# Performance work log

Hardware: AMD Instinct MI355X
Metric: run time of the kernel (lower is better)

## Reference

```python
import jax, jax.numpy as jnp
import numpy as np

INPUT_SIZE = 512
HIDDEN = 1024
N_QP = 64
M_QP = 128
QP_ITER = 50
MIN_EIG = 0.01
N_P = N_QP * (N_QP + 1) // 2              # 2080
N_H = M_QP * N_QP                          # 8192
N_OUT = N_P + N_QP + N_H + M_QP            # 10464
BATCH = 1024


def setup_inputs() -> dict:
    key = jax.random.key(0)
    ks = jax.random.split(key, 4)
    s = lambda fan_in: np.float32(1.0 / np.sqrt(fan_in))
    return {
        "x": jax.random.normal(ks[0], (BATCH, INPUT_SIZE), jnp.float32),
        "W1": jax.random.normal(ks[1], (INPUT_SIZE, HIDDEN), jnp.float32) * s(INPUT_SIZE),
        "b1": jnp.zeros((HIDDEN,), jnp.float32),
        "W2": jax.random.normal(ks[2], (HIDDEN, HIDDEN), jnp.float32) * s(HIDDEN),
        "b2": jnp.zeros((HIDDEN,), jnp.float32),
        "W3": jax.random.normal(ks[3], (HIDDEN, N_OUT), jnp.float32) * s(HIDDEN),
        "b3": jnp.zeros((N_OUT,), jnp.float32),
    }


def _make_psd(p):
    # p: (bs, n(n+1)/2) packed row-major lower triangle of Cholesky factor L.
    # Diagonal entries (index i(i+1)/2 - 1) -> sqrt(min_eig) + softplus, so P = L L' is PSD.
    bs = p.shape[0]
    i = jnp.arange(1, N_QP + 1)
    diag_idx = i * (i + 1) // 2 - 1
    p = p.at[:, diag_idx].set(np.float32(np.sqrt(MIN_EIG)) + jax.nn.softplus(p[:, diag_idx]))
    r, c = jnp.tril_indices(N_QP)
    L = jnp.zeros((bs, N_QP, N_QP), p.dtype).at[:, r, c].set(p)
    return jnp.einsum('bik,bjk->bij', L, L)


def _forward(x, W1, b1, W2, b2, W3, b3):
    # MLP generating QP parameters (P, q, H, b)
    h = jax.nn.relu(x @ W1 + b1)
    h = jax.nn.relu(h @ W2 + b2)
    out = h @ W3 + b3                               # (bs, N_OUT)
    P_params = out[:, :N_P]
    q = out[:, N_P:N_P + N_QP]                      # (bs, n)
    H = out[:, N_P + N_QP:N_P + N_QP + N_H].reshape(-1, M_QP, N_QP)  # (bs, m, n)
    b = out[:, N_P + N_QP + N_H:]                   # (bs, m)
    P = _make_psd(P_params)                         # (bs, n, n)

    # Step sizes: tau = sigma = 0.9 / ||H||_2, spectral norm via 10 fixed power iterations
    v = jnp.ones((x.shape[0], N_QP), x.dtype) / np.float32(np.sqrt(N_QP))
    for _ in range(10):
        w = jnp.einsum('bmn,bm->bn', H, jnp.einsum('bmn,bn->bm', H, v))
        v = w / (jnp.linalg.norm(w, axis=1, keepdims=True) + 1e-12)
    sn = jnp.linalg.norm(jnp.einsum('bmn,bn->bm', H, v), axis=1) + 1e-6
    tau = (0.9 / sn)[:, None]                       # (bs, 1) primal step
    sig = tau                                       # dual step

    # Precompute (I + tau P)^{-1} once; fixed across PDHG iterations
    eye = jnp.eye(N_QP, dtype=x.dtype)
    Minv = jnp.linalg.inv(eye[None] + tau[:, :, None] * P)

    x0 = jnp.zeros((x.shape[0], N_QP), x.dtype)
    lam0 = jnp.zeros((x.shape[0], M_QP), x.dtype)

    def step(carry, _):
        xp, xbar, lam = carry
        lam = jax.nn.relu(lam - sig * (jnp.einsum('bmn,bn->bm', H, xbar) + b))
        xn = jnp.einsum('bnk,bk->bn', Minv, xp + tau * (jnp.einsum('bmn,bm->bn', H, lam) - q))
        return (xn, 2.0 * xn - xp, lam), None

    (xs, _, _), _ = jax.lax.scan(step, (x0, x0, lam0), None, length=QP_ITER)
    return xs  # (bs, n_qp): last primal iterate, matching solver(...)[1][:, -1, :]


def reference(x, W1, b1, W2, b2, W3, b3):
    return _forward(x, W1, b1, W2, b2, W3, b3)
```

## Files before the change

### kernel.cpp

```cpp
#include <hip/hip_runtime.h>
#include <cstdint>

typedef unsigned short u16;
typedef __attribute__((ext_vector_type(8))) short short8;
typedef __attribute__((ext_vector_type(4))) float floatx4;
typedef __attribute__((ext_vector_type(4))) float f4;

#define NQP   64
#define MQP   128
#define NP    2080
#define NHH   8192
#define NOUT  10464
#define NOUTP 10496

__device__ __forceinline__ float b2f(u16 u) {
  union { unsigned int i; float f; } v; v.i = ((unsigned int)u) << 16; return v.f;
}
__device__ __forceinline__ u16 f2b(float f) {
  union { float f; unsigned int i; } v; v.f = f;
  unsigned int r = v.i + 0x7fffu + ((v.i >> 16) & 1u);
  return (u16)(r >> 16);
}

__global__ __launch_bounds__(256) void detect_dtype(const u16* __restrict__ w,
                                                    int* __restrict__ flag) {
  __shared__ int cnt;
  if (threadIdx.x == 0) cnt = 0;
  __syncthreads();
  int c = 0;
  for (int i = threadIdx.x; i < 16384; i += 256) {
    const int e = (w[i] >> 7) & 0xFF;
    if (e >= 130 || e <= 90) ++c;
  }
  atomicAdd(&cnt, c);
  __syncthreads();
  if (threadIdx.x == 0) flag[0] = (cnt > 3000) ? 1 : 0;
}

__device__ __forceinline__ u16 load_elem_bf16(const void* p, size_t idx, int isf32) {
  return isf32 ? f2b(((const float*)p)[idx]) : ((const u16*)p)[idx];
}

__global__ __launch_bounds__(256) void convert_bf16(const void* __restrict__ in,
                                                    u16* __restrict__ out, int n,
                                                    const int* __restrict__ flag) {
  const int isf = flag[0];
  for (int i = blockIdx.x * 256 + threadIdx.x; i < n; i += gridDim.x * 256)
    out[i] = load_elem_bf16(in, i, isf);
}

__global__ __launch_bounds__(256) void conv_biases(const void* __restrict__ b1,
                                                   const void* __restrict__ b2,
                                                   const void* __restrict__ b3,
                                                   float* __restrict__ bf1,
                                                   float* __restrict__ bf2,
                                                   float* __restrict__ bf3,
                                                   const int* __restrict__ flag) {
  const int isf = flag[0];
  const int i = blockIdx.x * 256 + threadIdx.x;
  if (i < 1024) {
    bf1[i] = isf ? ((const float*)b1)[i] : b2f(((const u16*)b1)[i]);
  } else if (i < 2048) {
    const int j = i - 1024;
    bf2[j] = isf ? ((const float*)b2)[j] : b2f(((const u16*)b2)[j]);
  } else if (i < 2048 + NOUT) {
    const int j = i - 2048;
    bf3[j] = isf ? ((const float*)b3)[j] : b2f(((const u16*)b3)[j]);
  }
}

__global__ __launch_bounds__(256) void transpose_all(const void* __restrict__ W1,
                                                     const void* __restrict__ W2,
                                                     const void* __restrict__ W3,
                                                     u16* __restrict__ W1t,
                                                     u16* __restrict__ W2t,
                                                     u16* __restrict__ W3t,
                                                     const int* __restrict__ flag) {
  const int bx = blockIdx.x, by = blockIdx.y;
  const void* in; u16* out; int K, N, Npad, bxo;
  if (bx < 32)      { in = W1; out = W1t; K = 512;  N = 1024; Npad = 1024;  bxo = 0;
                      if (by >= 16) return; }
  else if (bx < 64) { in = W2; out = W2t; K = 1024; N = 1024; Npad = 1024;  bxo = 32; }
  else              { in = W3; out = W3t; K = 1024; N = NOUT; Npad = NOUTP; bxo = 64; }
  __shared__ u16 tile[32][33];
  const int isf = flag[0];
  const int n0 = (bx - bxo) * 32, k0 = by * 32;
  const int tx = threadIdx.x & 31, ty = threadIdx.x >> 5;
#pragma unroll
  for (int i = 0; i < 4; ++i) {
    const int k = k0 + ty + 8 * i, n = n0 + tx;
    tile[ty + 8 * i][tx] = (n < N) ? load_elem_bf16(in, (size_t)k * N + n, isf) : (u16)0;
  }
  __syncthreads();
#pragma unroll
  for (int i = 0; i < 4; ++i) {
    const int n = n0 + ty + 8 * i, k = k0 + tx;
    if (n < Npad) out[(size_t)n * K + k] = tile[tx][ty + 8 * i];
  }
}

__device__ __forceinline__ void gload_lds16(const u16* g, u16* l) {
  __builtin_amdgcn_global_load_lds((const __attribute__((address_space(1))) void*)g,
                                   (__attribute__((address_space(3))) void*)l, 16, 0, 0);
}

template <int EPI, bool HAS_LO>
__global__ __launch_bounds__(256) void gemm_bt(const u16* __restrict__ Ahi, const u16* __restrict__ Alo,
                                               const u16* __restrict__ Bt,  const float* __restrict__ bias,
                                               u16* __restrict__ Chi, u16* __restrict__ Clo,
                                               float* __restrict__ Cf,
                                               int M, int N, int K) {
  __shared__ __align__(16) u16 lA[128 * 32];
  __shared__ __align__(16) u16 lAlo[128 * 32];
  __shared__ __align__(16) u16 lB[128 * 32];
  const int tile_n = blockIdx.x * 128;
  const int tile_m = blockIdx.y * 128;
  const int lane = threadIdx.x & 63;
  const int wv   = threadIdx.x >> 6;
  const int wm = (wv & 1) * 64;
  const int wn = (wv >> 1) * 64;
  const int sr = lane >> 2;
  const int sk = (lane & 3) * 8;
  floatx4 acc[4][4] = {};

  for (int k0 = 0; k0 < K; k0 += 32) {
#pragma unroll
    for (int it = 0; it < 2; ++it) {
      const int slot = it * 4 + wv;
      const int r = slot * 16 + sr;
      gload_lds16(Ahi + (size_t)(tile_m + r) * K + k0 + sk, lA + slot * 512);
      if (HAS_LO)
        gload_lds16(Alo + (size_t)(tile_m + r) * K + k0 + sk, lAlo + slot * 512);
      gload_lds16(Bt + (size_t)(tile_n + r) * K + k0 + sk, lB + slot * 512);
    }
    __syncthreads();
    const int ro = lane & 15;
    const int qo = (lane >> 4) * 8;
    short8 af[4], bfr[4], al[4];
#pragma unroll
    for (int i = 0; i < 4; ++i) af[i] = *(const short8*)(lA + (wm + i * 16 + ro) * 32 + qo);
#pragma unroll
    for (int j = 0; j < 4; ++j) bfr[j] = *(const short8*)(lB + (wn + j * 16 + ro) * 32 + qo);
    if (HAS_LO) {
#pragma unroll
      for (int i = 0; i < 4; ++i) al[i] = *(const short8*)(lAlo + (wm + i * 16 + ro) * 32 + qo);
    }
#pragma unroll
    for (int i = 0; i < 4; ++i)
#pragma unroll
      for (int j = 0; j < 4; ++j) {
        acc[i][j] = __builtin_amdgcn_mfma_f32_16x16x32_bf16(af[i], bfr[j], acc[i][j], 0, 0, 0);
        if (HAS_LO)
          acc[i][j] = __builtin_amdgcn_mfma_f32_16x16x32_bf16(al[i], bfr[j], acc[i][j], 0, 0, 0);
      }
    __syncthreads();
  }

  const int colb = tile_n + wn + (lane & 15);
  const int rowb = tile_m + wm + (lane >> 4) * 4;
#pragma unroll
  for (int j = 0; j < 4; ++j) {
    const int col = colb + j * 16;
    const float bv = (col < N) ? bias[col] : 0.f;
#pragma unroll
    for (int i = 0; i < 4; ++i) {
#pragma unroll
      for (int v = 0; v < 4; ++v) {
        const int row = rowb + i * 16 + v;
        float val = acc[i][j][v] + bv;
        if (EPI == 0) {
          val = fmaxf(val, 0.f);
          const u16 hi = f2b(val);
          const float lo = val - b2f(hi);
          Chi[(size_t)row * N + col] = hi;
          Clo[(size_t)row * N + col] = f2b(lo);
        } else if (EPI == 2) {
          val = fmaxf(val, 0.f);
          Chi[(size_t)row * N + col] = f2b(val);
        } else {
          if (col < N) Cf[(size_t)row * N + col] = val;
        }
      }
    }
  }
}

__device__ __forceinline__ f4 ld4s(const float* p) { return *(const f4*)p; }
__device__ __forceinline__ void st4s(float* p, f4 v) { *(f4*)p = v; }
__device__ __forceinline__ float dot4(f4 a, f4 b) {
  return fmaf(a.x, b.x, fmaf(a.y, b.y, fmaf(a.z, b.z, a.w * b.w)));
}
__device__ __forceinline__ f4 shx4(f4 v, int m) {
  f4 r;
  r.x = __shfl_xor(v.x, m, 64); r.y = __shfl_xor(v.y, m, 64);
  r.z = __shfl_xor(v.z, m, 64); r.w = __shfl_xor(v.w, m, 64);
  return r;
}
__device__ __forceinline__ int hQ(int m, int g) {
  return (m << 6) + (((g ^ (m & 15))) << 2);
}

__global__ __launch_bounds__(256, 4) void qp_solve(const float* __restrict__ outbuf,
                                                   void* __restrict__ xs,
                                                   const int* __restrict__ flag) {
  __shared__ __align__(16) float H_s[8192];
  __shared__ __align__(16) float b_s[128];
  __shared__ __align__(16) float part_s[4][64];
  __shared__ __align__(16) float xb_s[64];
  __shared__ __align__(16) float xp_s[2][64];
  __shared__ __align__(16) float q_s[64];
  __shared__ __align__(16) float buf2[2][64];

  const int t = threadIdx.x;
  const int w = t >> 6, l = t & 63;
  const int am = 32 * w + (l >> 1), as = l & 1;
  const int bg = l & 15, bc = l >> 4;
  const int bb2 = l & 48;
  const int ci = 16 * w + (l >> 2), cc = l & 3;
  const int isf = flag[0];
  const float* ob = outbuf + (size_t)blockIdx.x * NOUT;

  float* Ld = H_s;
  float* ps = H_s + 4352;
  for (int e = t; e < 4352; e += 256) Ld[e] = 0.f;
  for (int e = t; e < NP; e += 256) ps[e] = ob[e];
  if (t < 64) q_s[t] = ob[NP + t];
  if (t >= 128 && t < 256) b_s[t - 128] = ob[NP + NQP + NHH + (t - 128)];
  __syncthreads();
  if (t < 64) {
    const int i = t + 1;
    const int d = i * (i + 1) / 2 - 1;
    const float xv = ps[d];
    ps[d] = 0.1f + (fmaxf(xv, 0.f) + log1pf(expf(-fabsf(xv))));
  }
  __syncthreads();
  for (int e = t; e < NP; e += 256) {
    int i = (int)((sqrtf(8.f * (float)e + 1.f) - 1.f) * 0.5f);
    while ((i + 1) * (i + 2) / 2 <= e) ++i;
    while (i * (i + 1) / 2 > e) --i;
    const int j = e - i * (i + 1) / 2;
    Ld[i * 68 + j] = ps[e];
  }
  __syncthreads();

  float M[16];
#pragma unroll
  for (int jj = 0; jj < 16; ++jj) M[jj] = 0.f;
#pragma unroll
  for (int h = 0; h < 2; ++h) {
    f4 Lr[8];
#pragma unroll
    for (int g = 0; g < 8; ++g) Lr[g] = ld4s(&Ld[ci * 68 + (h * 8 + g) * 4]);
#pragma unroll
    for (int jj = 0; jj < 16; ++jj) {
      const int j = 16 * cc + jj;
      float s = 0.f;
#pragma unroll
      for (int g = 0; g < 8; ++g) s += dot4(Lr[g], ld4s(&Ld[j * 68 + (h * 8 + g) * 4]));
      M[jj] += s;
    }
  }
  __syncthreads();

  for (int e = t; e < NHH; e += 256) {
    const int m = e >> 6, n = e & 63;
    H_s[hQ(m, n >> 2) + (n & 3)] = ob[NP + NQP + e];
  }
  if (t < 64) xb_s[t] = 0.125f;
  __syncthreads();

  for (int pi = 0; pi < 10; ++pi) {
    float s = 0.f;
#pragma unroll
    for (int k = 0; k < 8; ++k) {
      const int g = 8 * as + k;
      s += dot4(ld4s(&H_s[hQ(am, g)]), ld4s(&xb_s[4 * g]));
    }
    s += __shfl_xor(s, 1, 64);
    {
      f4 u = {0.f, 0.f, 0.f, 0.f};
#pragma unroll
      for (int k = 0; k < 8; ++k) {
        const int m = 32 * w + 8 * bc + k;
        u += ld4s(&H_s[hQ(m, bg)]) * __shfl(s, bb2 + 2 * k, 64);
      }
      u += shx4(u, 16); u += shx4(u, 32);
      if (l < 16) st4s(&part_s[w][4 * bg], u);
    }
    __syncthreads();
    const float ut = (part_s[0][l] + part_s[1][l]) + (part_s[2][l] + part_s[3][l]);
    float ss = ut * ut;
#pragma unroll
    for (int o = 1; o <= 32; o <<= 1) ss += __shfl_xor(ss, o, 64);
    if (w == 0) xb_s[l] = ut / (sqrtf(ss) + 1e-12f);
    __syncthreads();
  }

  {
    float s = 0.f;
#pragma unroll
    for (int k = 0; k < 8; ++k) {
      const int g = 8 * as + k;
      s += dot4(ld4s(&H_s[hQ(am, g)]), ld4s(&xb_s[4 * g]));
    }
    s += __shfl_xor(s, 1, 64);
    float ss = as ? 0.f : s * s;
#pragma unroll
    for (int o = 1; o <= 32; o <<= 1) ss += __shfl_xor(ss, o, 64);
    if (l == 0) part_s[w][0] = ss;
  }
  __syncthreads();
  const float tau = 0.9f / (sqrtf(part_s[0][0] + part_s[1][0] + part_s[2][0] + part_s[3][0]) + 1e-6f);

#pragma unroll
  for (int jj = 0; jj < 16; ++jj)
    M[jj] = tau * M[jj] + ((16 * cc + jj == ci) ? 1.0f : 0.0f);

  if (ci == 0) {
#pragma unroll
    for (int jj = 0; jj < 16; ++jj) buf2[0][16 * cc + jj] = M[jj];
  }
  __syncthreads();
#pragma unroll
  for (int k = 0; k < 64; ++k) {
    const int kb = k & 1;
    const int kc = k >> 4;
    const float d = 1.0f / buf2[kb][k];
    f4 rv[4];
#pragma unroll
    for (int u = 0; u < 4; ++u) rv[u] = ld4s(&buf2[kb][16 * cc + 4 * u]);
    const float f = __shfl(M[k & 15], (l & 60) | kc, 64);
    if (ci == k) {
#pragma unroll
      for (int jj = 0; jj < 16; ++jj) M[jj] = rv[jj >> 2][jj & 3] * d;
      if (cc == kc) M[k & 15] = d;
    } else {
#pragma unroll
      for (int jj = 0; jj < 16; ++jj)
        M[jj] = fmaf(-f, rv[jj >> 2][jj & 3] * d, M[jj]);
      if (cc == kc) M[k & 15] = -f * d;
    }
    if (k < 63 && ci == k + 1) {
#pragma unroll
      for (int jj = 0; jj < 16; ++jj) buf2[1 - kb][16 * cc + jj] = M[jj];
    }
    __syncthreads();
  }

  float c0;
  {
    float acc = 0.f;
#pragma unroll
    for (int u = 0; u < 4; ++u) {
      const f4 qv = ld4s(&q_s[16 * cc + 4 * u]);
      acc = fmaf(M[4 * u + 0], qv.x, acc);
      acc = fmaf(M[4 * u + 1], qv.y, acc);
      acc = fmaf(M[4 * u + 2], qv.z, acc);
      acc = fmaf(M[4 * u + 3], qv.w, acc);
    }
    acc += __shfl_xor(acc, 1, 64);
    acc += __shfl_xor(acc, 2, 64);
    c0 = tau * acc;
  }

  if (t < 64) { xb_s[t] = 0.f; xp_s[0][t] = 0.f; }
  float lam = 0.f, xpr = 0.f;
  const float br = b_s[am];
  __syncthreads();

  for (int it = 0; it < 50; ++it) {
    float s = 0.f;
#pragma unroll
    for (int k = 0; k < 8; ++k) {
      const int g = 8 * as + k;
      s += dot4(ld4s(&H_s[hQ(am, g)]), ld4s(&xb_s[4 * g]));
    }
    s += __shfl_xor(s, 1, 64);
    lam = fmaxf(lam - tau * (s + br), 0.f);
    {
      f4 u = {0.f, 0.f, 0.f, 0.f};
#pragma unroll
      for (int k = 0; k < 8; ++k) {
        const int m = 32 * w + 8 * bc + k;
        u += ld4s(&H_s[hQ(m, bg)]) * __shfl(lam, bb2 + 2 * k, 64);
      }
      u += shx4(u, 16); u += shx4(u, 32);
      if (l < 16) st4s(&part_s[w][4 * bg], u);
    }
    __syncthreads();
    const float* xrd = xp_s[it & 1];
    float* xwr = xp_s[1 - (it & 1)];
    float acc = 0.f;
#pragma unroll
    for (int u = 0; u < 4; ++u) {
      const int base = 16 * cc + 4 * u;
      const f4 pv = (ld4s(&part_s[0][base]) + ld4s(&part_s[1][base])) +
                    (ld4s(&part_s[2][base]) + ld4s(&part_s[3][base]));
      const f4 rv = ld4s(&xrd[base]) + pv * tau;
      acc = fmaf(M[4 * u + 0], rv.x, acc);
      acc = fmaf(M[4 * u + 1], rv.y, acc);
      acc = fmaf(M[4 * u + 2], rv.z, acc);
      acc = fmaf(M[4 * u + 3], rv.w, acc);
    }
    acc += __shfl_xor(acc, 1, 64);
    acc += __shfl_xor(acc, 2, 64);
    if (cc == 0) {
      const float xn = acc - c0;
      xwr[ci] = xn;
      xb_s[ci] = 2.f * xn - xpr;
      xpr = xn;
    }
    __syncthreads();
  }

  if (cc == 0) {
    const size_t oi = (size_t)blockIdx.x * NQP + ci;
    if (isf) ((float*)xs)[oi] = xpr;
    else     ((u16*)xs)[oi]   = f2b(xpr);
  }
}

extern "C" void kernel_launch(void* const* d_in, const int* in_sizes, int n_in,
                              void* d_out, int out_size, void* d_ws, size_t ws_size,
                              hipStream_t stream) {
  const void* x  = d_in[0];
  const void* W1 = d_in[1];
  const void* b1 = d_in[2];
  const void* W2 = d_in[3];
  const void* b2 = d_in[4];
  const void* W3 = d_in[5];
  const void* b3 = d_in[6];

  char* ws = (char*)d_ws;
  size_t off = 0;
  auto take = [&](size_t bytes) -> char* {
    char* r = ws + off;
    off += (bytes + 255) & ~(size_t)255;
    return r;
  };
  int*   flag = (int*)take(256);
  float* bf1  = (float*)take(1024 * 4);
  float* bf2  = (float*)take(1024 * 4);
  float* bf3  = (float*)take((size_t)NOUT * 4);
  u16*   W3t  = (u16*)take((size_t)NOUTP * 1024 * 2);
  u16*   h2hi = (u16*)take(1024ull * 1024 * 2);
  char*  region = take(1024ull * NOUT * 4);
  float* outf = (float*)region;
  u16* xb   = (u16*)(region + 0);
  u16* W1t  = (u16*)(region + (1u << 20));
  u16* W2t  = (u16*)(region + (2u << 20));
  u16* h1hi = (u16*)(region + (4u << 20));
  u16* h1lo = (u16*)(region + (6u << 20));
  (void)ws_size; (void)in_sizes; (void)n_in; (void)out_size;

  detect_dtype<<<dim3(1), 256, 0, stream>>>((const u16*)W1, flag);

  convert_bf16<<<dim3(512), 256, 0, stream>>>(x, xb, 1024 * 512, flag);
  conv_biases<<<dim3(49), 256, 0, stream>>>(b1, b2, b3, bf1, bf2, bf3, flag);
  transpose_all<<<dim3(392, 32), 256, 0, stream>>>(W1, W2, W3, W1t, W2t, W3t, flag);

  gemm_bt<0, false><<<dim3(8, 8), 256, 0, stream>>>(xb, nullptr, W1t, bf1,
                                                    h1hi, h1lo, nullptr, 1024, 1024, 512);
  gemm_bt<2, true><<<dim3(8, 8), 256, 0, stream>>>(h1hi, h1lo, W2t, bf2,
                                                   h2hi, nullptr, nullptr, 1024, 1024, 1024);
  gemm_bt<1, false><<<dim3(NOUTP / 128, 8), 256, 0, stream>>>(h2hi, nullptr, W3t, bf3,
                                                              nullptr, nullptr, outf, 1024, NOUT, 1024);
  qp_solve<<<dim3(1024), 256, 0, stream>>>(outf, d_out, flag);
}
```

Before: 511.4 us.

## Keep H rows and columns in registers instead of shared memory in QP solver

Each thread now loads its slice of H directly from global memory into registers, once as row fragments for H·x and once as column fragments for Hᵀ·λ. λ is broadcast through a small shared array rather than cross-lane shuffles. This removes the 32KB shared H tile, its swizzled indexing and the per-iteration shared loads and shuffle reductions. The cost is about 64 extra VGPRs per thread and strided global loads for the column fragments. The Gauss-Jordan inverse loop is also restructured to load pivot rows inside a single unrolled loop with a predicate.

```diff
diff --git a/kernel.cpp b/kernel.cpp
--- a/kernel.cpp
+++ b/kernel.cpp
@@ -186,25 +186,15 @@
 }
 
 __device__ __forceinline__ f4 ld4s(const float* p) { return *(const f4*)p; }
-__device__ __forceinline__ void st4s(float* p, f4 v) { *(f4*)p = v; }
 __device__ __forceinline__ float dot4(f4 a, f4 b) {
   return fmaf(a.x, b.x, fmaf(a.y, b.y, fmaf(a.z, b.z, a.w * b.w)));
-}
-__device__ __forceinline__ f4 shx4(f4 v, int m) {
-  f4 r;
-  r.x = __shfl_xor(v.x, m, 64); r.y = __shfl_xor(v.y, m, 64);
-  r.z = __shfl_xor(v.z, m, 64); r.w = __shfl_xor(v.w, m, 64);
-  return r;
-}
-__device__ __forceinline__ int hQ(int m, int g) {
-  return (m << 6) + (((g ^ (m & 15))) << 2);
 }
 
 __global__ __launch_bounds__(256, 4) void qp_solve(const float* __restrict__ outbuf,
                                                    void* __restrict__ xs,
                                                    const int* __restrict__ flag) {
-  __shared__ __align__(16) float H_s[8192];
-  __shared__ __align__(16) float b_s[128];
+  __shared__ __align__(16) float LS[6432];
+  __shared__ __align__(16) float lam_s[128];
   __shared__ __align__(16) float part_s[4][64];
   __shared__ __align__(16) float xb_s[64];
   __shared__ __align__(16) float xp_s[2][64];
@@ -214,18 +204,16 @@
   const int t = threadIdx.x;
   const int w = t >> 6, l = t & 63;
   const int am = 32 * w + (l >> 1), as = l & 1;
-  const int bg = l & 15, bc = l >> 4;
-  const int bb2 = l & 48;
   const int ci = 16 * w + (l >> 2), cc = l & 3;
   const int isf = flag[0];
   const float* ob = outbuf + (size_t)blockIdx.x * NOUT;
-
-  float* Ld = H_s;
-  float* ps = H_s + 4352;
+  const float* Hg = ob + (NP + NQP);
+
+  float* Ld = LS;
+  float* ps = LS + 4352;
   for (int e = t; e < 4352; e += 256) Ld[e] = 0.f;
   for (int e = t; e < NP; e += 256) ps[e] = ob[e];
   if (t < 64) q_s[t] = ob[NP + t];
-  if (t >= 128 && t < 256) b_s[t - 128] = ob[NP + NQP + NHH + (t - 128)];
   __syncthreads();
   if (t < 64) {
     const int i = t + 1;
@@ -260,33 +248,38 @@
       M[jj] += s;
     }
   }
-  __syncthreads();
-
-  for (int e = t; e < NHH; e += 256) {
-    const int m = e >> 6, n = e & 63;
-    H_s[hQ(m, n >> 2) + (n & 3)] = ob[NP + NQP + e];
-  }
+
+  f4 hrow[8];
+#pragma unroll
+  for (int k = 0; k < 8; ++k)
+    hrow[k] = *(const f4*)(Hg + (size_t)am * 64 + 32 * as + 4 * k);
+  f4 hcol[8];
+#pragma unroll
+  for (int u = 0; u < 8; ++u) {
+    f4 c;
+    c.x = Hg[(32 * w + 4 * u + 0) * 64 + l];
+    c.y = Hg[(32 * w + 4 * u + 1) * 64 + l];
+    c.z = Hg[(32 * w + 4 * u + 2) * 64 + l];
+    c.w = Hg[(32 * w + 4 * u + 3) * 64 + l];
+    hcol[u] = c;
+  }
+  const float br = ob[NP + NQP + NHH + am];
+
   if (t < 64) xb_s[t] = 0.125f;
   __syncthreads();
 
   for (int pi = 0; pi < 10; ++pi) {
     float s = 0.f;
 #pragma unroll
-    for (int k = 0; k < 8; ++k) {
-      const int g = 8 * as + k;
-      s += dot4(ld4s(&H_s[hQ(am, g)]), ld4s(&xb_s[4 * g]));
-    }
+    for (int k = 0; k < 8; ++k)
+      s += dot4(hrow[k], ld4s(&xb_s[32 * as + 4 * k]));
     s += __shfl_xor(s, 1, 64);
-    {
-      f4 u = {0.f, 0.f, 0.f, 0.f};
-#pragma unroll
-      for (int k = 0; k < 8; ++k) {
-        const int m = 32 * w + 8 * bc + k;
-        u += ld4s(&H_s[hQ(m, bg)]) * __shfl(s, bb2 + 2 * k, 64);
-      }
-      u += shx4(u, 16); u += shx4(u, 32);
-      if (l < 16) st4s(&part_s[w][4 * bg], u);
-    }
+    if (as == 0) lam_s[am] = s;
+    float ua = 0.f;
+#pragma unroll
+    for (int u = 0; u < 8; ++u)
+      ua += dot4(hcol[u], ld4s(&lam_s[32 * w + 4 * u]));
+    part_s[w][l] = ua;
     __syncthreads();
     const float ut = (part_s[0][l] + part_s[1][l]) + (part_s[2][l] + part_s[3][l]);
     float ss = ut * ut;
@@ -299,10 +292,8 @@
   {
     float s = 0.f;
 #pragma unroll
-    for (int k = 0; k < 8; ++k) {
-      const int g = 8 * as + k;
-      s += dot4(ld4s(&H_s[hQ(am, g)]), ld4s(&xb_s[4 * g]));
-    }
+    for (int k = 0; k < 8; ++k)
+      s += dot4(hrow[k], ld4s(&xb_s[32 * as + 4 * k]));
     s += __shfl_xor(s, 1, 64);
     float ss = as ? 0.f : s * s;
 #pragma unroll
@@ -326,20 +317,24 @@
     const int kb = k & 1;
     const int kc = k >> 4;
     const float d = 1.0f / buf2[kb][k];
-    f4 rv[4];
-#pragma unroll
-    for (int u = 0; u < 4; ++u) rv[u] = ld4s(&buf2[kb][16 * cc + 4 * u]);
     const float f = __shfl(M[k & 15], (l & 60) | kc, 64);
-    if (ci == k) {
-#pragma unroll
-      for (int jj = 0; jj < 16; ++jj) M[jj] = rv[jj >> 2][jj & 3] * d;
-      if (cc == kc) M[k & 15] = d;
-    } else {
-#pragma unroll
-      for (int jj = 0; jj < 16; ++jj)
-        M[jj] = fmaf(-f, rv[jj >> 2][jj & 3] * d, M[jj]);
-      if (cc == kc) M[k & 15] = -f * d;
-    }
+    const bool piv = (ci == k);
+#pragma unroll
+    for (int u = 0; u < 4; ++u) {
+      const f4 rv = ld4s(&buf2[kb][16 * cc + 4 * u]);
+      if (piv) {
+        M[4 * u + 0] = rv.x * d;
+        M[4 * u + 1] = rv.y * d;
+        M[4 * u + 2] = rv.z * d;
+        M[4 * u + 3] = rv.w * d;
+      } else {
+        M[4 * u + 0] = fmaf(-f, rv.x * d, M[4 * u + 0]);
+        M[4 * u + 1] = fmaf(-f, rv.y * d, M[4 * u + 1]);
+        M[4 * u + 2] = fmaf(-f, rv.z * d, M[4 * u + 2]);
+        M[4 * u + 3] = fmaf(-f, rv.w * d, M[4 * u + 3]);
+      }
+    }
+    if (cc == kc) M[k & 15] = piv ? d : -f * d;
     if (k < 63 && ci == k + 1) {
 #pragma unroll
       for (int jj = 0; jj < 16; ++jj) buf2[1 - kb][16 * cc + jj] = M[jj];
@@ -365,28 +360,21 @@
 
   if (t < 64) { xb_s[t] = 0.f; xp_s[0][t] = 0.f; }
   float lam = 0.f, xpr = 0.f;
-  const float br = b_s[am];
   __syncthreads();
 
   for (int it = 0; it < 50; ++it) {
     float s = 0.f;
 #pragma unroll
-    for (int k = 0; k < 8; ++k) {
-      const int g = 8 * as + k;
-      s += dot4(ld4s(&H_s[hQ(am, g)]), ld4s(&xb_s[4 * g]));
-    }
+    for (int k = 0; k < 8; ++k)
+      s += dot4(hrow[k], ld4s(&xb_s[32 * as + 4 * k]));
     s += __shfl_xor(s, 1, 64);
     lam = fmaxf(lam - tau * (s + br), 0.f);
-    {
-      f4 u = {0.f, 0.f, 0.f, 0.f};
-#pragma unroll
-      for (int k = 0; k < 8; ++k) {
-        const int m = 32 * w + 8 * bc + k;
-        u += ld4s(&H_s[hQ(m, bg)]) * __shfl(lam, bb2 + 2 * k, 64);
-      }
-      u += shx4(u, 16); u += shx4(u, 32);
-      if (l < 16) st4s(&part_s[w][4 * bg], u);
-    }
+    if (as == 0) lam_s[am] = lam;
+    float ua = 0.f;
+#pragma unroll
+    for (int u = 0; u < 8; ++u)
+      ua += dot4(hcol[u], ld4s(&lam_s[32 * w + 4 * u]));
+    part_s[w][l] = ua;
     __syncthreads();
     const float* xrd = xp_s[it & 1];
     float* xwr = xp_s[1 - (it & 1)];
```

Result: slower. 1.636 ms (+219.8%).
